# Optimization experiments

Hardware: AMD Instinct MI355X
Metric: run time of the kernel (lower is better)

## Reference

```python
import jax, jax.numpy as jnp
import numpy as np
from functools import partial

B, N = 4, 4096
WIDTH, HEADS, HD = 768, 12, 64
MINI, CONV_W = 16, 4
TTT_BASE_LR = 1.0
THETA = 10000.0
EPS = 1e-6


def _rope_table():
    half = HD // 2
    freqs = 1.0 / THETA ** (np.arange(0, HD, 2)[:half].astype(np.float32) / HD)
    t = np.arange(2 * MINI)
    f = np.outer(t, freqs).astype(np.float32)
    return jnp.asarray(np.cos(f)), jnp.asarray(np.sin(f))

_COS, _SIN = _rope_table()


def apply_rope(x, cos, sin):
    # x: [B,N,H,HD]; cos/sin: [N, HD//2]; pairs are (x[2i], x[2i+1])
    xe, xo = x[..., 0::2], x[..., 1::2]
    c, s = cos[None, :, None, :], sin[None, :, None, :]
    return jnp.stack([xe * c - xo * s, xe * s + xo * c], axis=-1).reshape(x.shape)


def ln_fwd(x, g, b):
    mu = x.mean(-1, keepdims=True)
    std = jnp.sqrt(x.var(-1, keepdims=True) + EPS)
    return g * ((x - mu) / std) + b


def ln_fused_l2_bwd(x, target, g, b):
    # grad of 0.5*||LN(x)-target||^2 w.r.t. x (official TTT fused form)
    D = x.shape[-1]
    mu = x.mean(-1, keepdims=True)
    std = jnp.sqrt(x.var(-1, keepdims=True) + EPS)
    x_hat = (x - mu) / std
    gxh = ((g * x_hat + b) - target) * g
    return (D * gxh - gxh.sum(-1, keepdims=True)
            - x_hat * (gxh * x_hat).sum(-1, keepdims=True)) / (D * std)


def causal_dwconv(x, kernel, bias):
    # depthwise causal conv: x [B,N,C], kernel [W,1,C], left-pad W-1
    y = jax.lax.conv_general_dilated(
        x, kernel, (1,), [(CONV_W - 1, 0)],
        dimension_numbers=('NWC', 'WIO', 'NWC'), feature_group_count=WIDTH)
    return y + bias


def _mini_step(ln_g, ln_b, carry, inp):
    W1, b1h = carry
    XQ, XK, XV, eta = inp  # [m,hd] x3, eta [m,m]
    Z1 = XK @ W1 + b1h
    grad = ln_fused_l2_bwd(Z1, XV - XK, ln_g, ln_b)
    Attn = jnp.tril(XQ @ XK.T)
    b1_bar = b1h - jnp.tril(eta) @ grad
    Z1_bar = XQ @ W1 - (eta * Attn) @ grad + b1_bar
    last_eta = eta[-1][:, None]
    W1_new = W1 - (last_eta * XK).T @ grad
    b1_new = b1h - jnp.sum(last_eta * grad, axis=0, keepdims=True)
    out = XQ + ln_fwd(Z1_bar, ln_g, ln_b)
    return (W1_new, b1_new), out


def ttt_forward(hidden_states, wq, wv, wo, wg,
                conv_q_kernel, conv_q_bias, conv_k_kernel, conv_k_bias,
                W1, b1, ttt_norm_scale, ttt_norm_bias,
                lr_kernel, lr_bias, learnable_token_idx,
                post_norm_scale, post_norm_bias):
    Bsz, Nlen, _ = hidden_states.shape
    xqk = hidden_states @ wq
    XV = hidden_states @ wv
    XQ = causal_dwconv(xqk, conv_q_kernel, conv_q_bias)
    XK = causal_dwconv(xqk, conv_k_kernel, conv_k_bias)
    XQ = XQ.reshape(Bsz, Nlen, HEADS, HD)
    XK = XK.reshape(Bsz, Nlen, HEADS, HD)
    XV = XV.reshape(Bsz, Nlen, HEADS, HD)

    pos = jnp.arange(Nlen) % MINI  # RoPE restarts each mini-batch (official)
    XQ = apply_rope(XQ, _COS[pos], _SIN[pos])
    XK = apply_rope(XK, _COS[pos], _SIN[pos])

    def to_mb(x):  # [B,N,H,hd] -> [B,H,n_mini,mini,hd]
        return x.reshape(Bsz, -1, MINI, HEADS, HD).transpose(0, 3, 1, 2, 4)
    XQ, XK, XV = to_mb(XQ), to_mb(XK), to_mb(XV)

    # learnable per-head, per-token learning rate -> eta [B,H,n_mini,mini,mini]
    X_mb = hidden_states.reshape(Bsz, -1, MINI, WIDTH)
    ttt_lr = jax.nn.sigmoid(jnp.einsum('bnmw,hw->bhnm', X_mb, lr_kernel[..., 0])
                            + lr_bias[None, :, None, :])
    ttt_lr = TTT_BASE_LR * ttt_lr / HD
    token_idx = jnp.maximum(1.0 / jnp.arange(1, MINI + 1, dtype=jnp.float32)
                            + learnable_token_idx, 0.0)
    eta = token_idx[None, None, None, :, None] * ttt_lr[:, :, :, None, :]

    def per_head(xq, xk, xv, e, w1, b1h, g, bln):
        step = partial(_mini_step, g, bln)
        _, out = jax.lax.scan(step, (w1, b1h), (xq, xk, xv, e))
        return out.reshape(-1, HD)  # [N, hd]

    per_batch = jax.vmap(per_head, in_axes=(0, 0, 0, 0, 0, 0, 0, 0))
    out = jax.vmap(per_batch, in_axes=(0, 0, 0, 0, None, None, None, None))(
        XQ, XK, XV, eta, W1, b1, ttt_norm_scale, ttt_norm_bias)  # [B,H,N,hd]
    out = out.transpose(0, 2, 1, 3).reshape(Bsz, Nlen, WIDTH)

    z = ln_fwd(out, post_norm_scale, post_norm_bias)  # post_norm
    gate = jax.nn.gelu(hidden_states @ wg)            # GLU gating
    return (gate * z) @ wo


def setup_inputs() -> dict:
    key = jax.random.key(0)
    ks = jax.random.split(key, 12)
    std = 0.02
    f32 = jnp.float32
    return {
        'hidden_states': jax.random.normal(ks[0], (B, N, WIDTH), f32),
        'wq': jax.random.normal(ks[1], (WIDTH, HEADS * HD), f32) * std,
        'wv': jax.random.normal(ks[2], (WIDTH, HEADS * HD), f32) * std,
        'wo': jax.random.normal(ks[3], (WIDTH, WIDTH), f32) * std,
        'wg': jax.random.normal(ks[4], (WIDTH, WIDTH), f32) * std,
        'conv_q_kernel': jax.random.normal(ks[5], (CONV_W, 1, WIDTH), f32) * 0.5,
        'conv_q_bias': jnp.zeros((WIDTH,), f32),
        'conv_k_kernel': jax.random.normal(ks[6], (CONV_W, 1, WIDTH), f32) * 0.5,
        'conv_k_bias': jnp.zeros((WIDTH,), f32),
        'W1': jax.random.normal(ks[7], (HEADS, HD, HD), f32) * std,
        'b1': jnp.zeros((HEADS, 1, HD), f32),
        'ttt_norm_scale': jnp.ones((HEADS, HD), f32),
        'ttt_norm_bias': jnp.zeros((HEADS, HD), f32),
        'lr_kernel': jax.random.normal(ks[8], (HEADS, WIDTH, 1), f32) * std,
        'lr_bias': jnp.zeros((HEADS, 1), f32),
        'learnable_token_idx': jax.random.normal(ks[9], (MINI,), f32) * 0.01,
        'post_norm_scale': jnp.ones((WIDTH,), f32),
        'post_norm_bias': jnp.zeros((WIDTH,), f32),
    }


def reference(hidden_states, wq, wv, wo, wg, conv_q_kernel, conv_q_bias,
              conv_k_kernel, conv_k_bias, W1, b1, ttt_norm_scale, ttt_norm_bias,
              lr_kernel, lr_bias, learnable_token_idx, post_norm_scale, post_norm_bias):
    return ttt_forward(hidden_states, wq, wv, wo, wg, conv_q_kernel, conv_q_bias,
                       conv_k_kernel, conv_k_bias, W1, b1, ttt_norm_scale,
                       ttt_norm_bias, lr_kernel, lr_bias, learnable_token_idx,
                       post_norm_scale, post_norm_bias)
```

## Files before the change

kernel.cpp:

```cpp
#include <hip/hip_runtime.h>
#include <math.h>

#define WIDTH 768
#define HEADS 12
#define HD 64
#define MINI 16
#define NSEQ 4096
#define BATCH 4
#define NMB (NSEQ/MINI)
#define EPS 1e-6f

typedef __attribute__((ext_vector_type(8))) short bf16x8;
typedef __attribute__((ext_vector_type(4))) float f32x4;
typedef __attribute__((ext_vector_type(4))) int   i32x4;

__device__ __forceinline__ float bfu2f(unsigned short h) {
    return __uint_as_float(((unsigned)h) << 16);
}
__device__ __forceinline__ void tsplit(float f, unsigned short& h, unsigned short& l) {
    unsigned uh = __float_as_uint(f) & 0xffff0000u;
    h = (unsigned short)(uh >> 16);
    l = (unsigned short)(__float_as_uint(f - __uint_as_float(uh)) >> 16);
}
__device__ __forceinline__ unsigned tpack(float f) {
    unsigned uh = __float_as_uint(f) & 0xffff0000u;
    return uh | (__float_as_uint(f - __uint_as_float(uh)) >> 16);
}
__device__ __forceinline__ void barrier_lgkm() {
    asm volatile("s_waitcnt lgkmcnt(0)\n\ts_barrier" ::: "memory");
}

struct ScanSM {
    unsigned sXKp[16 * 68];
    unsigned sGE[16 * 68];
    unsigned sCB[16 * 20];
    float    sU[64 * 68];
    float    sRedM[16 * 36];
    float    sRed3[16 * 36];
    float    sB1d[64];
};
struct GemmSM {
    unsigned short sAh[128 * 40], sAl[128 * 40];
    unsigned short sBh[128 * 40], sBl[128 * 40];
};
struct WtSM { float sT[64][65]; };
#define SMEM_BYTES 40960

__device__ void wtconv_body(char* smraw, int n0, int k0, const float* __restrict__ w,
                            unsigned short* __restrict__ hiT, unsigned short* __restrict__ loT)
{
    WtSM* W = (WtSM*)smraw;
    int t = threadIdx.x, r = t >> 2, cs = (t & 3) * 16;
#pragma unroll
    for (int i = 0; i < 16; i += 4)
        *(float4*)&W->sT[r][cs + i] = *(const float4*)&w[(size_t)(k0 + r) * WIDTH + n0 + cs + i];
    __syncthreads();
    ushort4 hb[4], lb[4];
#pragma unroll
    for (int i = 0; i < 16; i++) {
        unsigned short hh, ll;
        tsplit(W->sT[cs + i][r], hh, ll);
        ((unsigned short*)hb)[i] = hh;
        ((unsigned short*)lb)[i] = ll;
    }
#pragma unroll
    for (int i = 0; i < 4; i++) {
        *(ushort4*)&hiT[(size_t)(n0 + r) * WIDTH + k0 + cs + i * 4] = hb[i];
        *(ushort4*)&loT[(size_t)(n0 + r) * WIDTH + k0 + cs + i * 4] = lb[i];
    }
}

template<int ACT, int SPLITA>
__device__ void gemm_body(char* smraw, int by,
                          const float* __restrict__ Af,
                          const unsigned short* __restrict__ APh,
                          const unsigned short* __restrict__ APl,
                          const unsigned short* __restrict__ BhT,
                          const unsigned short* __restrict__ BlT,
                          float* __restrict__ C, int ldc, int K)
{
    GemmSM* g = (GemmSM*)smraw;
    const int tid = threadIdx.x;
    const int bm = by * 128;
    const int w = tid >> 6, lane = tid & 63, quad = lane >> 4, m16 = lane & 15;
    const int mw = (w & 1) * 64, nw = (w >> 1) * 64;
    const int srow = tid >> 1, sseg = (tid & 1) * 16;
    f32x4 acc[4][4];
#pragma unroll
    for (int a = 0; a < 4; a++)
#pragma unroll
        for (int c = 0; c < 4; c++) acc[a][c] = (f32x4){0.f, 0.f, 0.f, 0.f};

    for (int k0 = 0; k0 < K; k0 += 32) {
        uint4 vb0 = *(const uint4*)(BhT + (size_t)srow * K + k0 + sseg);
        uint4 vb1 = *(const uint4*)(BhT + (size_t)srow * K + k0 + sseg + 8);
        uint4 vd0 = *(const uint4*)(BlT + (size_t)srow * K + k0 + sseg);
        uint4 vd1 = *(const uint4*)(BlT + (size_t)srow * K + k0 + sseg + 8);
        if (SPLITA) {
            const float* Ap = Af + (size_t)(bm + srow) * K + k0 + sseg;
            float4 f0 = *(const float4*)(Ap);
            float4 f1 = *(const float4*)(Ap + 4);
            float4 f2 = *(const float4*)(Ap + 8);
            float4 f3 = *(const float4*)(Ap + 12);
            __syncthreads();
            unsigned short hs[16], ls[16];
            float fv[16] = {f0.x, f0.y, f0.z, f0.w, f1.x, f1.y, f1.z, f1.w,
                            f2.x, f2.y, f2.z, f2.w, f3.x, f3.y, f3.z, f3.w};
#pragma unroll
            for (int i = 0; i < 16; i++) tsplit(fv[i], hs[i], ls[i]);
            *(uint4*)&g->sAh[srow * 40 + sseg]     = *(uint4*)&hs[0];
            *(uint4*)&g->sAh[srow * 40 + sseg + 8] = *(uint4*)&hs[8];
            *(uint4*)&g->sAl[srow * 40 + sseg]     = *(uint4*)&ls[0];
            *(uint4*)&g->sAl[srow * 40 + sseg + 8] = *(uint4*)&ls[8];
        } else {
            uint4 va0 = *(const uint4*)(APh + (size_t)(bm + srow) * K + k0 + sseg);
            uint4 va1 = *(const uint4*)(APh + (size_t)(bm + srow) * K + k0 + sseg + 8);
            uint4 vc0 = *(const uint4*)(APl + (size_t)(bm + srow) * K + k0 + sseg);
            uint4 vc1 = *(const uint4*)(APl + (size_t)(bm + srow) * K + k0 + sseg + 8);
            __syncthreads();
            *(uint4*)&g->sAh[srow * 40 + sseg] = va0; *(uint4*)&g->sAh[srow * 40 + sseg + 8] = va1;
            *(uint4*)&g->sAl[srow * 40 + sseg] = vc0; *(uint4*)&g->sAl[srow * 40 + sseg + 8] = vc1;
        }
        *(uint4*)&g->sBh[srow * 40 + sseg] = vb0; *(uint4*)&g->sBh[srow * 40 + sseg + 8] = vb1;
        *(uint4*)&g->sBl[srow * 40 + sseg] = vd0; *(uint4*)&g->sBl[srow * 40 + sseg + 8] = vd1;
        __syncthreads();
        bf16x8 ah[4], al[4];
#pragma unroll
        for (int mt = 0; mt < 4; mt++) {
            ah[mt] = *(const bf16x8*)&g->sAh[(mw + mt * 16 + m16) * 40 + quad * 8];
            al[mt] = *(const bf16x8*)&g->sAl[(mw + mt * 16 + m16) * 40 + quad * 8];
        }
#pragma unroll
        for (int nt = 0; nt < 4; nt++) {
            bf16x8 bh8 = *(const bf16x8*)&g->sBh[(nw + nt * 16 + m16) * 40 + quad * 8];
            bf16x8 bl8 = *(const bf16x8*)&g->sBl[(nw + nt * 16 + m16) * 40 + quad * 8];
#pragma unroll
            for (int mt = 0; mt < 4; mt++) {
                acc[mt][nt] = __builtin_amdgcn_mfma_f32_16x16x32_bf16(ah[mt], bh8, acc[mt][nt], 0, 0, 0);
                acc[mt][nt] = __builtin_amdgcn_mfma_f32_16x16x32_bf16(al[mt], bh8, acc[mt][nt], 0, 0, 0);
                acc[mt][nt] = __builtin_amdgcn_mfma_f32_16x16x32_bf16(ah[mt], bl8, acc[mt][nt], 0, 0, 0);
            }
        }
    }
#pragma unroll
    for (int mt = 0; mt < 4; mt++)
#pragma unroll
        for (int nt = 0; nt < 4; nt++)
#pragma unroll
            for (int r = 0; r < 4; r++) {
                float v = acc[mt][nt][r];
                if (ACT == 1) {
                    float inner = 0.7978845608028654f * (v + 0.044715f * v * v * v);
                    v = 0.5f * v * (1.0f + tanhf(inner));
                }
                C[(size_t)(bm + mw + mt * 16 + quad * 4 + r) * ldc + nw + nt * 16 + m16] = v;
            }
}

__device__ void scan_body(char* smraw, int bh,
    const unsigned short* __restrict__ XQh, const unsigned short* __restrict__ XQl,
    const unsigned short* __restrict__ XKh, const unsigned short* __restrict__ XKl,
    const float* __restrict__ XVb, const float* __restrict__ lr_buf,
    const float* __restrict__ W1g, const float* __restrict__ b1g,
    const float* __restrict__ gln, const float* __restrict__ blnv,
    const float* __restrict__ lti, float* __restrict__ out)
{
    ScanSM* S = (ScanSM*)smraw;
    const int tid = threadIdx.x;
    const int w = tid >> 6, lane = tid & 63;
    const int quad = lane >> 4, m16 = lane & 15;
    const int b = bh / HEADS, h = bh - b * HEADS;
    const int jc = 16 * w + m16;
    const int j4 = 16 * w + quad * 4;

    float g4[4], b4[4], b1v[4], gg4[4];
#pragma unroll
    for (int r = 0; r < 4; r++) {
        g4[r] = gln[h * 64 + j4 + r];
        b4[r] = blnv[h * 64 + j4 + r];
        b1v[r] = b1g[h * 64 + j4 + r];
        gg4[r] = g4[r] * g4[r];
    }
    const float tok15 = fmaxf(1.0f / 16.0f + lti[15], 0.0f);
    float tki[4];
#pragma unroll
    for (int r = 0; r < 4; r++)
        tki[r] = fmaxf(1.0f / (float)(quad * 4 + r + 1) + lti[quad * 4 + r], 0.0f) / tok15;

    float ags = (gg4[0] + gg4[1]) + (gg4[2] + gg4[3]);
    ags += __shfl_xor(ags, 16); ags += __shfl_xor(ags, 32);
    if (lane == 0) S->sB1d[w] = ags;
    __syncthreads();
    const float Ag2 = S->sB1d[0] + S->sB1d[1] + S->sB1d[2] + S->sB1d[3];

    float W1f[2][8]; bf16x8 w1h[2], w1l[2];
#pragma unroll
    for (int kt = 0; kt < 2; kt++)
#pragma unroll
        for (int e = 0; e < 8; e++) {
            float f = W1g[h * 4096 + (kt * 32 + quad * 8 + e) * 64 + jc];
            W1f[kt][e] = f;
            unsigned short hh, ll; tsplit(f, hh, ll);
            w1h[kt][e] = (short)hh; w1l[kt][e] = (short)ll;
        }

    const unsigned short* xqh = XQh + (size_t)bh * NSEQ * 64;
    const unsigned short* xql = XQl + (size_t)bh * NSEQ * 64;
    const unsigned short* xkh = XKh + (size_t)bh * NSEQ * 64;
    const unsigned short* xkl = XKl + (size_t)bh * NSEQ * 64;
    const float* xvB = XVb + (size_t)b * NSEQ * WIDTH + h * 64;
    const float* lrB = lr_buf + (size_t)bh * NSEQ;
    float* outB = out + (size_t)b * NSEQ * WIDTH + h * 64;

    bf16x8 ones8;
#pragma unroll
    for (int e = 0; e < 8; e++) ones8[e] = (short)0x3F80;
    const bf16x8 zf = {0, 0, 0, 0, 0, 0, 0, 0};

    bf16x8 pqh[2], pql[2], pkh[2], pkl[2];
    float4 pxv; ushort4 pth, ptl, poh, pol; float plr;
    {
        const size_t tok = m16;
#pragma unroll
        for (int kt = 0; kt < 2; kt++) {
            pqh[kt] = *(const bf16x8*)(xqh + tok * 64 + kt * 32 + quad * 8);
            pql[kt] = *(const bf16x8*)(xql + tok * 64 + kt * 32 + quad * 8);
            pkh[kt] = *(const bf16x8*)(xkh + tok * 64 + kt * 32 + quad * 8);
            pkl[kt] = *(const bf16x8*)(xkl + tok * 64 + kt * 32 + quad * 8);
        }
        pxv = *(const float4*)(xvB + tok * WIDTH + j4);
        pth = *(const ushort4*)(xkh + tok * 64 + j4);
        ptl = *(const ushort4*)(xkl + tok * 64 + j4);
        poh = *(const ushort4*)(xqh + tok * 64 + j4);
        pol = *(const ushort4*)(xql + tok * 64 + j4);
        plr = lrB[m16];
    }

    for (int s = 0; s < NMB; s++) {
        bf16x8 qh[2] = {pqh[0], pqh[1]}, ql[2] = {pql[0], pql[1]};
        bf16x8 kh[2] = {pkh[0], pkh[1]}, kl[2] = {pkl[0], pkl[1]};
        float xv4[4] = {pxv.x, pxv.y, pxv.z, pxv.w};
        float xkt4[4], xqo4[4];
        xkt4[0] = bfu2f(pth.x) + bfu2f(ptl.x); xkt4[1] = bfu2f(pth.y) + bfu2f(ptl.y);
        xkt4[2] = bfu2f(pth.z) + bfu2f(ptl.z); xkt4[3] = bfu2f(pth.w) + bfu2f(ptl.w);
        xqo4[0] = bfu2f(poh.x) + bfu2f(pol.x); xqo4[1] = bfu2f(poh.y) + bfu2f(pol.y);
        xqo4[2] = bfu2f(poh.z) + bfu2f(pol.z); xqo4[3] = bfu2f(poh.w) + bfu2f(pol.w);
        const float lrc = plr;
        const float sc = tok15 * lrc;

#pragma unroll
        for (int kt = 0; kt < 2; kt++) {
            i32x4 p0, p1;
#pragma unroll
            for (int e = 0; e < 4; e++)
                p0[e] = (int)((((unsigned)(unsigned short)kh[kt][e]) << 16) | (unsigned short)kl[kt][e]);
#pragma unroll
            for (int e = 0; e < 4; e++)
                p1[e] = (int)((((unsigned)(unsigned short)kh[kt][4 + e]) << 16) | (unsigned short)kl[kt][4 + e]);
            *(i32x4*)&S->sXKp[m16 * 68 + kt * 32 + quad * 8] = p0;
            *(i32x4*)&S->sXKp[m16 * 68 + kt * 32 + quad * 8 + 4] = p1;
        }

        {
            const int sn = (s + 1 < NMB) ? s + 1 : s;
            const size_t tok = (size_t)sn * 16 + m16;
#pragma unroll
            for (int kt = 0; kt < 2; kt++) {
                pqh[kt] = *(const bf16x8*)(xqh + tok * 64 + kt * 32 + quad * 8);
                pql[kt] = *(const bf16x8*)(xql + tok * 64 + kt * 32 + quad * 8);
                pkh[kt] = *(const bf16x8*)(xkh + tok * 64 + kt * 32 + quad * 8);
                pkl[kt] = *(const bf16x8*)(xkl + tok * 64 + kt * 32 + quad * 8);
            }
            pxv = *(const float4*)(xvB + tok * WIDTH + j4);
            pth = *(const ushort4*)(xkh + tok * 64 + j4);
            ptl = *(const ushort4*)(xkl + tok * 64 + j4);
            poh = *(const ushort4*)(xqh + tok * 64 + j4);
            pol = *(const ushort4*)(xql + tok * 64 + j4);
            plr = lrB[(size_t)sn * 16 + m16];
        }

        f32x4 z1 = {0.f, 0.f, 0.f, 0.f}, zq = {0.f, 0.f, 0.f, 0.f};
#pragma unroll
        for (int kt = 0; kt < 2; kt++) {
            z1 = __builtin_amdgcn_mfma_f32_16x16x32_bf16(w1h[kt], kh[kt], z1, 0, 0, 0);
            z1 = __builtin_amdgcn_mfma_f32_16x16x32_bf16(w1h[kt], kl[kt], z1, 0, 0, 0);
            z1 = __builtin_amdgcn_mfma_f32_16x16x32_bf16(w1l[kt], kh[kt], z1, 0, 0, 0);
            zq = __builtin_amdgcn_mfma_f32_16x16x32_bf16(w1h[kt], qh[kt], zq, 0, 0, 0);
            zq = __builtin_amdgcn_mfma_f32_16x16x32_bf16(w1h[kt], ql[kt], zq, 0, 0, 0);
            zq = __builtin_amdgcn_mfma_f32_16x16x32_bf16(w1l[kt], qh[kt], zq, 0, 0, 0);
        }
        f32x4 at = {0.f, 0.f, 0.f, 0.f};
        if (w == 3) {
#pragma unroll
            for (int kt = 0; kt < 2; kt++) {
                at = __builtin_amdgcn_mfma_f32_16x16x32_bf16(qh[kt], kh[kt], at, 0, 0, 0);
                at = __builtin_amdgcn_mfma_f32_16x16x32_bf16(qh[kt], kl[kt], at, 0, 0, 0);
                at = __builtin_amdgcn_mfma_f32_16x16x32_bf16(ql[kt], kh[kt], at, 0, 0, 0);
            }
        }
#pragma unroll
        for (int r = 0; r < 4; r++) z1[r] += b1v[r];

        float c1g[4];
        float s1 = 0.f, s2 = 0.f, a1 = 0.f, a4 = 0.f, a3 = 0.f, a5 = 0.f;
#pragma unroll
        for (int r = 0; r < 4; r++) {
            float z = z1[r];
            float t = xv4[r] - xkt4[r];
            c1g[r] = (b4[r] - t) * g4[r];
            s1 += z; s2 += z * z;
            float gz = gg4[r] * z;
            a1 += gz; a4 += gz * z;
            a3 += c1g[r]; a5 += c1g[r] * z;
        }
        s1 += __shfl_xor(s1, 16); s2 += __shfl_xor(s2, 16);
        a1 += __shfl_xor(a1, 16); a4 += __shfl_xor(a4, 16);
        a3 += __shfl_xor(a3, 16); a5 += __shfl_xor(a5, 16);
        s1 += __shfl_xor(s1, 32); s2 += __shfl_xor(s2, 32);
        a1 += __shfl_xor(a1, 32); a4 += __shfl_xor(a4, 32);
        a3 += __shfl_xor(a3, 32); a5 += __shfl_xor(a5, 32);
        if (quad == 0) {
            *(float4*)&S->sRedM[m16 * 36 + w * 8]     = make_float4(s1, s2, a1, a4);
            *(float4*)&S->sRedM[m16 * 36 + w * 8 + 4] = make_float4(a3, a5, 0.f, 0.f);
        }
        if (w == 3) {
            i32x4 cw;
#pragma unroll
            for (int r = 0; r < 4; r++) {
                float v = (m16 <= quad * 4 + r) ? -(tki[r] * (1.0f + at[r])) : 0.0f;
                cw[r] = (int)tpack(v);
            }
            *(i32x4*)&S->sCB[m16 * 20 + quad * 4] = cw;
        }
        barrier_lgkm();

        float S1 = 0.f, S2 = 0.f, A1 = 0.f, A4 = 0.f, A3 = 0.f, A5 = 0.f;
#pragma unroll
        for (int w2 = 0; w2 < 4; w2++) {
            float4 pa = *(const float4*)&S->sRedM[m16 * 36 + w2 * 8];
            float4 pb = *(const float4*)&S->sRedM[m16 * 36 + w2 * 8 + 4];
            S1 += pa.x; S2 += pa.y; A1 += pa.z; A4 += pa.w;
            A3 += pb.x; A5 += pb.y;
        }
        float mu = S1 * (1.0f / 64.0f);
        float var = S2 * (1.0f / 64.0f) - mu * mu;
        float rstd = rsqrtf(var + EPS);
        float T1 = rstd * (A1 - mu * Ag2) + A3;
        float T2 = rstd * rstd * (A4 - 2.0f * mu * A1 + mu * mu * Ag2)
                 + rstd * (A5 - mu * A3);
        i32x4 gw;
#pragma unroll
        for (int r = 0; r < 4; r++) {
            float xh = (z1[r] - mu) * rstd;
            float gxh = gg4[r] * xh + c1g[r];
            float grad = (64.0f * gxh - T1 - xh * T2) * (rstd * (1.0f / 64.0f));
            gw[r] = (int)tpack(sc * grad);
        }
        *(i32x4*)&S->sGE[m16 * 68 + j4] = gw;
        barrier_lgkm();

        bf16x8 akh8 = zf, akl8 = zf;
#pragma unroll
        for (int e = 0; e < 8; e++) {
            unsigned u = (quad < 2) ? S->sXKp[(quad * 8 + e) * 68 + 16 * w + m16] : 0u;
            akh8[e] = (short)(u >> 16); akl8[e] = (short)(u & 0xffffu);
        }
        bf16x8 agh = zf, agl = zf;
#pragma unroll
        for (int nt = 0; nt < 4; nt++) {
            bf16x8 gh8 = zf, gl8 = zf;
#pragma unroll
            for (int e = 0; e < 8; e++) {
                unsigned u = (quad < 2) ? S->sGE[(quad * 8 + e) * 68 + 16 * nt + m16] : 0u;
                gh8[e] = (short)(u >> 16); gl8[e] = (short)(u & 0xffffu);
            }
            if (nt == w) { agh = gh8; agl = gl8; }
            f32x4 ua = {0.f, 0.f, 0.f, 0.f};
            ua = __builtin_amdgcn_mfma_f32_16x16x32_bf16(akh8, gh8, ua, 0, 0, 0);
            ua = __builtin_amdgcn_mfma_f32_16x16x32_bf16(akl8, gh8, ua, 0, 0, 0);
            ua = __builtin_amdgcn_mfma_f32_16x16x32_bf16(akh8, gl8, ua, 0, 0, 0);
#pragma unroll
            for (int r = 0; r < 4; r++)
                S->sU[(16 * w + quad * 4 + r) * 68 + 16 * nt + m16] = ua[r];
            if (w == 1) {
                f32x4 bda = {0.f, 0.f, 0.f, 0.f};
                bda = __builtin_amdgcn_mfma_f32_16x16x32_bf16(ones8, gh8, bda, 0, 0, 0);
                bda = __builtin_amdgcn_mfma_f32_16x16x32_bf16(ones8, gl8, bda, 0, 0, 0);
                if (quad == 0) S->sB1d[16 * nt + m16] = bda[0];
            }
        }
        bf16x8 cbh = zf, cbl = zf;
#pragma unroll
        for (int e = 0; e < 8; e++) {
            unsigned u = (quad < 2) ? S->sCB[(quad * 8 + e) * 20 + m16] : 0u;
            cbh[e] = (short)(u >> 16); cbl[e] = (short)(u & 0xffffu);
        }
        zq = __builtin_amdgcn_mfma_f32_16x16x32_bf16(agh, cbh, zq, 0, 0, 0);
        zq = __builtin_amdgcn_mfma_f32_16x16x32_bf16(agl, cbh, zq, 0, 0, 0);
        zq = __builtin_amdgcn_mfma_f32_16x16x32_bf16(agh, cbl, zq, 0, 0, 0);
        float zb[4];
#pragma unroll
        for (int r = 0; r < 4; r++) zb[r] = zq[r] + b1v[r];
        float u1p = (zb[0] + zb[1]) + (zb[2] + zb[3]);
        float u2p = (zb[0] * zb[0] + zb[1] * zb[1]) + (zb[2] * zb[2] + zb[3] * zb[3]);
        u1p += __shfl_xor(u1p, 16); u2p += __shfl_xor(u2p, 16);
        u1p += __shfl_xor(u1p, 32); u2p += __shfl_xor(u2p, 32);
        if (quad == 0) *(float2*)&S->sRed3[m16 * 36 + w * 8] = make_float2(u1p, u2p);
        barrier_lgkm();

        float V1 = 0.f, V2 = 0.f;
#pragma unroll
        for (int w2 = 0; w2 < 4; w2++) {
            float2 p = *(const float2*)&S->sRed3[m16 * 36 + w2 * 8];
            V1 += p.x; V2 += p.y;
        }
        float mu2 = V1 * (1.0f / 64.0f);
        float va2 = V2 * (1.0f / 64.0f) - mu2 * mu2;
        float rs2 = rsqrtf(va2 + EPS);
        float4 ov;
        ov.x = xqo4[0] + fmaf(g4[0], (zb[0] - mu2) * rs2, b4[0]);
        ov.y = xqo4[1] + fmaf(g4[1], (zb[1] - mu2) * rs2, b4[1]);
        ov.z = xqo4[2] + fmaf(g4[2], (zb[2] - mu2) * rs2, b4[2]);
        ov.w = xqo4[3] + fmaf(g4[3], (zb[3] - mu2) * rs2, b4[3]);
        *(float4*)&outB[(size_t)(s * 16 + m16) * WIDTH + j4] = ov;

#pragma unroll
        for (int kt = 0; kt < 2; kt++)
#pragma unroll
            for (int e = 0; e < 8; e++) {
                float f = W1f[kt][e] - S->sU[(kt * 32 + quad * 8 + e) * 68 + jc];
                W1f[kt][e] = f;
                unsigned short hh, ll; tsplit(f, hh, ll);
                w1h[kt][e] = (short)hh; w1l[kt][e] = (short)ll;
            }
        float4 bdv = *(const float4*)&S->sB1d[j4];
        b1v[0] -= bdv.x; b1v[1] -= bdv.y; b1v[2] -= bdv.z; b1v[3] -= bdv.w;
    }
}

__global__ __launch_bounds__(256, 2)
void mega_kernel(const unsigned short* __restrict__ XQh, const unsigned short* __restrict__ XQl,
                 const unsigned short* __restrict__ XKh, const unsigned short* __restrict__ XKl,
                 const float* __restrict__ XVb, const float* __restrict__ lrbuf,
                 const float* __restrict__ W1, const float* __restrict__ b1,
                 const float* __restrict__ tns, const float* __restrict__ tnb,
                 const float* __restrict__ lti, float* __restrict__ ttto,
                 const float* __restrict__ wo, unsigned short* __restrict__ woThi,
                 unsigned short* __restrict__ woTlo,
                 const float* __restrict__ hidden, const unsigned short* __restrict__ wTgh,
                 const unsigned short* __restrict__ wTgl, float* __restrict__ gate)
{
    __shared__ __align__(16) char sm[SMEM_BYTES];
    int bid = blockIdx.x;
    if (bid < 48) {
        scan_body(sm, bid, XQh, XQl, XKh, XKl, XVb, lrbuf, W1, b1, tns, tnb, lti, ttto);
    } else if (bid < 192) {
        int idx = bid - 48;
        wtconv_body(sm, (idx % 12) * 64, (idx / 12) * 64, wo, woThi, woTlo);
    } else {
        int idx = bid - 192;
        int bx = idx % 6, by = idx / 6;
        int bn = bx * 128;
        gemm_body<1, 1>(sm, by, hidden, nullptr, nullptr,
                        wTgh + (size_t)bn * WIDTH, wTgl + (size_t)bn * WIDTH,
                        gate + bn, WIDTH, WIDTH);
    }
}

__global__ __launch_bounds__(256, 2)
void gemm_qv_kernel(const float* __restrict__ hidden,
                    const unsigned short* __restrict__ wThi, const unsigned short* __restrict__ wTlo,
                    float* __restrict__ xqk, float* __restrict__ XVb)
{
    __shared__ __align__(16) char sm[SMEM_BYTES];
    int bn = blockIdx.x * 128;
    float* C = (bn < WIDTH) ? (xqk + bn) : (XVb + bn - WIDTH);
    gemm_body<0, 1>(sm, blockIdx.y, hidden, nullptr, nullptr,
                    wThi + (size_t)bn * WIDTH, wTlo + (size_t)bn * WIDTH, C, WIDTH, WIDTH);
}

__global__ __launch_bounds__(256, 2)
void gemm_out_kernel(const unsigned short* __restrict__ gzh, const unsigned short* __restrict__ gzl,
                     const unsigned short* __restrict__ woThi, const unsigned short* __restrict__ woTlo,
                     float* __restrict__ out)
{
    __shared__ __align__(16) char sm[SMEM_BYTES];
    int bn = blockIdx.x * 128;
    gemm_body<0, 0>(sm, blockIdx.y, nullptr, gzh, gzl,
                    woThi + (size_t)bn * WIDTH, woTlo + (size_t)bn * WIDTH, out + bn, WIDTH, WIDTH);
}

__global__ __launch_bounds__(256)
void wtconv3_kernel(const float* __restrict__ wq, const float* __restrict__ wv,
                    const float* __restrict__ wg,
                    unsigned short* __restrict__ hiT, unsigned short* __restrict__ loT)
{
    __shared__ __align__(16) char sm[sizeof(WtSM)];
    int widx = blockIdx.z;
    const float* src = (widx == 0) ? wq : ((widx == 1) ? wv : wg);
    size_t off = (size_t)widx * WIDTH * WIDTH;
    wtconv_body(sm, blockIdx.x * 64, blockIdx.y * 64, src, hiT + off, loT + off);
}

__global__ __launch_bounds__(384)
void conv_rope_kernel(const float* __restrict__ xqk,
                      const float* __restrict__ kq, const float* __restrict__ bq,
                      const float* __restrict__ kk, const float* __restrict__ bk,
                      unsigned short* __restrict__ XQh, unsigned short* __restrict__ XQl,
                      unsigned short* __restrict__ XKh, unsigned short* __restrict__ XKl)
{
    int bid = blockIdx.x;
    int n = bid & (NSEQ - 1);
    int b = bid >> 12;
    int p = threadIdx.x;
    int c = p * 2;
    int pp = p & 31;
    float qe = bq[c], qo = bq[c + 1], ke = bk[c], ko = bk[c + 1];
#pragma unroll
    for (int w = 0; w < 4; w++) {
        int nn = n - 3 + w;
        if (nn >= 0) {
            const float* xr = xqk + ((size_t)(bid - n + nn)) * WIDTH + c;
            float xe = xr[0], xo = xr[1];
            qe = fmaf(xe, kq[w * WIDTH + c], qe);
            qo = fmaf(xo, kq[w * WIDTH + c + 1], qo);
            ke = fmaf(xe, kk[w * WIDTH + c], ke);
            ko = fmaf(xo, kk[w * WIDTH + c + 1], ko);
        }
    }
    int pos = n & (MINI - 1);
    float freq = expf(-(float)pp * (9.210340371976184f / 32.0f));
    float ang = (float)pos * freq;
    float c_ = cosf(ang), s_ = sinf(ang);
    int hh = p >> 5;
    int cc = pp * 2;
    size_t o = ((size_t)(b * HEADS + hh) * NSEQ + n) * 64 + cc;
    float q0 = qe * c_ - qo * s_, q1 = qe * s_ + qo * c_;
    float k0 = ke * c_ - ko * s_, k1 = ke * s_ + ko * c_;
    ushort2 h2, l2;
    tsplit(q0, h2.x, l2.x); tsplit(q1, h2.y, l2.y);
    *(ushort2*)&XQh[o] = h2; *(ushort2*)&XQl[o] = l2;
    tsplit(k0, h2.x, l2.x); tsplit(k1, h2.y, l2.y);
    *(ushort2*)&XKh[o] = h2; *(ushort2*)&XKl[o] = l2;
}

__global__ __launch_bounds__(256)
void lr_kernel(const float* __restrict__ hidden, const float* __restrict__ lrk,
               const float* __restrict__ lrb, float* __restrict__ lr_buf)
{
    int wave = threadIdx.x >> 6;
    int lane = threadIdx.x & 63;
    int row = blockIdx.x * 4 + wave;
    int b = row >> 12;
    int n = row & (NSEQ - 1);
    const float* hr = hidden + (size_t)row * WIDTH;
    float hv[12];
#pragma unroll
    for (int t = 0; t < 12; t++) hv[t] = hr[lane + 64 * t];
    for (int h = 0; h < HEADS; h++) {
        const float* lk = lrk + h * WIDTH;
        float acc = 0.f;
#pragma unroll
        for (int t = 0; t < 12; t++) acc = fmaf(hv[t], lk[lane + 64 * t], acc);
#pragma unroll
        for (int m = 1; m < 64; m <<= 1) acc += __shfl_xor(acc, m);
        if (lane == 0) {
            float s = 1.0f / (1.0f + __expf(-(acc + lrb[h])));
            lr_buf[((size_t)(b * HEADS + h)) * NSEQ + n] = s * (1.0f / HD);
        }
    }
}

__global__ __launch_bounds__(256)
void postgate_kernel(const float* __restrict__ tout, const float* __restrict__ gate,
                     const float* __restrict__ ps, const float* __restrict__ pb,
                     unsigned short* __restrict__ gzh, unsigned short* __restrict__ gzl)
{
    __shared__ float red[8];
    int row = blockIdx.x;
    int tid = threadIdx.x;
    const float* x = tout + (size_t)row * WIDTH;
    float v[3];
    float s1 = 0, s2 = 0;
#pragma unroll
// ... 80 lines not shown
```

Before: 1.163 ms.

## Run each TTT scan head on a single wavefront to remove block barriers

The sequential mini-batch scan for each (batch, head) now runs on one 64-lane wavefront instead of four waves splitting the 64 output columns. Each lane holds all four column tiles of W1 in registers and performs the full LN reductions with shuffles, so the per-step cross-wave LDS reductions and block barriers become plain lgkmcnt waits. MFMA sections are given higher scheduling priority, and the mega kernel's launch bounds drop to one block per SM. The trade-off is four times more MFMA and VALU work per wave on the serial critical path, much higher register pressure that may cause spills, and lower occupancy for the co-scheduled GEMM and weight-conversion blocks.

```diff
diff --git a/kernel.cpp b/kernel.cpp
--- a/kernel.cpp
+++ b/kernel.cpp
@@ -26,17 +26,16 @@
     unsigned uh = __float_as_uint(f) & 0xffff0000u;
     return uh | (__float_as_uint(f - __uint_as_float(uh)) >> 16);
 }
-__device__ __forceinline__ void barrier_lgkm() {
-    asm volatile("s_waitcnt lgkmcnt(0)\n\ts_barrier" ::: "memory");
-}
-
-struct ScanSM {
+__device__ __forceinline__ void fence_lds() {
+    asm volatile("s_waitcnt lgkmcnt(0)" ::: "memory");
+    __builtin_amdgcn_sched_barrier(0);
+}
+
+struct ScanSM1 {
     unsigned sXKp[16 * 68];
     unsigned sGE[16 * 68];
     unsigned sCB[16 * 20];
-    float    sU[64 * 68];
-    float    sRedM[16 * 36];
-    float    sRed3[16 * 36];
+    float    sUw[64 * 68];
     float    sB1d[64];
 };
 struct GemmSM {
@@ -46,11 +45,11 @@
 struct WtSM { float sT[64][65]; };
 #define SMEM_BYTES 40960
 
-__device__ void wtconv_body(char* smraw, int n0, int k0, const float* __restrict__ w,
+__device__ void wtconv_body(char* smraw, int tid, int n0, int k0, const float* __restrict__ w,
                             unsigned short* __restrict__ hiT, unsigned short* __restrict__ loT)
 {
     WtSM* W = (WtSM*)smraw;
-    int t = threadIdx.x, r = t >> 2, cs = (t & 3) * 16;
+    int t = tid, r = t >> 2, cs = (t & 3) * 16;
 #pragma unroll
     for (int i = 0; i < 16; i += 4)
         *(float4*)&W->sT[r][cs + i] = *(const float4*)&w[(size_t)(k0 + r) * WIDTH + n0 + cs + i];
@@ -71,7 +70,7 @@
 }
 
 template<int ACT, int SPLITA>
-__device__ void gemm_body(char* smraw, int by,
+__device__ void gemm_body(char* smraw, int tid, int by,
                           const float* __restrict__ Af,
                           const unsigned short* __restrict__ APh,
                           const unsigned short* __restrict__ APl,
@@ -80,7 +79,6 @@
                           float* __restrict__ C, int ldc, int K)
 {
     GemmSM* g = (GemmSM*)smraw;
-    const int tid = threadIdx.x;
     const int bm = by * 128;
     const int w = tid >> 6, lane = tid & 63, quad = lane >> 4, m16 = lane & 15;
     const int mw = (w & 1) * 64, nw = (w >> 1) * 64;
@@ -157,7 +155,7 @@
             }
 }
 
-__device__ void scan_body(char* smraw, int bh,
+__device__ void scan_wave(char* smraw, int lane, int bh,
     const unsigned short* __restrict__ XQh, const unsigned short* __restrict__ XQl,
     const unsigned short* __restrict__ XKh, const unsigned short* __restrict__ XKl,
     const float* __restrict__ XVb, const float* __restrict__ lr_buf,
@@ -165,44 +163,46 @@
     const float* __restrict__ gln, const float* __restrict__ blnv,
     const float* __restrict__ lti, float* __restrict__ out)
 {
-    ScanSM* S = (ScanSM*)smraw;
-    const int tid = threadIdx.x;
-    const int w = tid >> 6, lane = tid & 63;
+    ScanSM1* S = (ScanSM1*)smraw;
     const int quad = lane >> 4, m16 = lane & 15;
     const int b = bh / HEADS, h = bh - b * HEADS;
-    const int jc = 16 * w + m16;
-    const int j4 = 16 * w + quad * 4;
-
-    float g4[4], b4[4], b1v[4], gg4[4];
-#pragma unroll
-    for (int r = 0; r < 4; r++) {
-        g4[r] = gln[h * 64 + j4 + r];
-        b4[r] = blnv[h * 64 + j4 + r];
-        b1v[r] = b1g[h * 64 + j4 + r];
-        gg4[r] = g4[r] * g4[r];
-    }
+
+    float g4[4][4], b4[4][4], gg4[4][4], b1v[4][4];
+#pragma unroll
+    for (int jt = 0; jt < 4; jt++)
+#pragma unroll
+        for (int r = 0; r < 4; r++) {
+            int j = 16 * jt + quad * 4 + r;
+            g4[jt][r] = gln[h * 64 + j];
+            b4[jt][r] = blnv[h * 64 + j];
+            b1v[jt][r] = b1g[h * 64 + j];
+            gg4[jt][r] = g4[jt][r] * g4[jt][r];
+        }
     const float tok15 = fmaxf(1.0f / 16.0f + lti[15], 0.0f);
     float tki[4];
 #pragma unroll
     for (int r = 0; r < 4; r++)
         tki[r] = fmaxf(1.0f / (float)(quad * 4 + r + 1) + lti[quad * 4 + r], 0.0f) / tok15;
 
-    float ags = (gg4[0] + gg4[1]) + (gg4[2] + gg4[3]);
+    float ags = 0.f;
+#pragma unroll
+    for (int jt = 0; jt < 4; jt++)
+        ags += (gg4[jt][0] + gg4[jt][1]) + (gg4[jt][2] + gg4[jt][3]);
     ags += __shfl_xor(ags, 16); ags += __shfl_xor(ags, 32);
-    if (lane == 0) S->sB1d[w] = ags;
-    __syncthreads();
-    const float Ag2 = S->sB1d[0] + S->sB1d[1] + S->sB1d[2] + S->sB1d[3];
-
-    float W1f[2][8]; bf16x8 w1h[2], w1l[2];
-#pragma unroll
-    for (int kt = 0; kt < 2; kt++)
-#pragma unroll
-        for (int e = 0; e < 8; e++) {
-            float f = W1g[h * 4096 + (kt * 32 + quad * 8 + e) * 64 + jc];
-            W1f[kt][e] = f;
-            unsigned short hh, ll; tsplit(f, hh, ll);
-            w1h[kt][e] = (short)hh; w1l[kt][e] = (short)ll;
-        }
+    const float Ag2 = ags;
+
+    float W1f[4][2][8]; bf16x8 w1h[4][2], w1l[4][2];
+#pragma unroll
+    for (int jt = 0; jt < 4; jt++)
+#pragma unroll
+        for (int kt = 0; kt < 2; kt++)
+#pragma unroll
+            for (int e = 0; e < 8; e++) {
+                float f = W1g[h * 4096 + (kt * 32 + quad * 8 + e) * 64 + 16 * jt + m16];
+                W1f[jt][kt][e] = f;
+                unsigned short hh, ll; tsplit(f, hh, ll);
+                w1h[jt][kt][e] = (short)hh; w1l[jt][kt][e] = (short)ll;
+            }
 
     const unsigned short* xqh = XQh + (size_t)bh * NSEQ * 64;
     const unsigned short* xql = XQl + (size_t)bh * NSEQ * 64;
@@ -215,10 +215,9 @@
     bf16x8 ones8;
 #pragma unroll
     for (int e = 0; e < 8; e++) ones8[e] = (short)0x3F80;
-    const bf16x8 zf = {0, 0, 0, 0, 0, 0, 0, 0};
 
     bf16x8 pqh[2], pql[2], pkh[2], pkl[2];
-    float4 pxv; ushort4 pth, ptl, poh, pol; float plr;
+    float4 pxv[4]; ushort4 pth[4], ptl[4]; float plr;
     {
         const size_t tok = m16;
 #pragma unroll
@@ -228,25 +227,29 @@
             pkh[kt] = *(const bf16x8*)(xkh + tok * 64 + kt * 32 + quad * 8);
             pkl[kt] = *(const bf16x8*)(xkl + tok * 64 + kt * 32 + quad * 8);
         }
-        pxv = *(const float4*)(xvB + tok * WIDTH + j4);
-        pth = *(const ushort4*)(xkh + tok * 64 + j4);
-        ptl = *(const ushort4*)(xkl + tok * 64 + j4);
-        poh = *(const ushort4*)(xqh + tok * 64 + j4);
-        pol = *(const ushort4*)(xql + tok * 64 + j4);
+#pragma unroll
+        for (int jt = 0; jt < 4; jt++) {
+            pxv[jt] = *(const float4*)(xvB + tok * WIDTH + 16 * jt + quad * 4);
+            pth[jt] = *(const ushort4*)(xkh + tok * 64 + 16 * jt + quad * 4);
+            ptl[jt] = *(const ushort4*)(xkl + tok * 64 + 16 * jt + quad * 4);
+        }
         plr = lrB[m16];
     }
 
     for (int s = 0; s < NMB; s++) {
         bf16x8 qh[2] = {pqh[0], pqh[1]}, ql[2] = {pql[0], pql[1]};
         bf16x8 kh[2] = {pkh[0], pkh[1]}, kl[2] = {pkl[0], pkl[1]};
-        float xv4[4] = {pxv.x, pxv.y, pxv.z, pxv.w};
-        float xkt4[4], xqo4[4];
-        xkt4[0] = bfu2f(pth.x) + bfu2f(ptl.x); xkt4[1] = bfu2f(pth.y) + bfu2f(ptl.y);
-        xkt4[2] = bfu2f(pth.z) + bfu2f(ptl.z); xkt4[3] = bfu2f(pth.w) + bfu2f(ptl.w);
-        xqo4[0] = bfu2f(poh.x) + bfu2f(pol.x); xqo4[1] = bfu2f(poh.y) + bfu2f(pol.y);
-        xqo4[2] = bfu2f(poh.z) + bfu2f(pol.z); xqo4[3] = bfu2f(poh.w) + bfu2f(pol.w);
-        const float lrc = plr;
-        const float sc = tok15 * lrc;
+        float xv[4][4], xkt[4][4];
+#pragma unroll
+        for (int jt = 0; jt < 4; jt++) {
+            xv[jt][0] = pxv[jt].x; xv[jt][1] = pxv[jt].y;
+            xv[jt][2] = pxv[jt].z; xv[jt][3] = pxv[jt].w;
+            xkt[jt][0] = bfu2f(pth[jt].x) + bfu2f(ptl[jt].x);
+            xkt[jt][1] = bfu2f(pth[jt].y) + bfu2f(ptl[jt].y);
+            xkt[jt][2] = bfu2f(pth[jt].z) + bfu2f(ptl[jt].z);
+            xkt[jt][3] = bfu2f(pth[jt].w) + bfu2f(ptl[jt].w);
+        }
+        const float sc = tok15 * plr;
 
 #pragma unroll
         for (int kt = 0; kt < 2; kt++) {
@@ -271,59 +274,87 @@
                 pkh[kt] = *(const bf16x8*)(xkh + tok * 64 + kt * 32 + quad * 8);
                 pkl[kt] = *(const bf16x8*)(xkl + tok * 64 + kt * 32 + quad * 8);
             }
-            pxv = *(const float4*)(xvB + tok * WIDTH + j4);
-            pth = *(const ushort4*)(xkh + tok * 64 + j4);
-            ptl = *(const ushort4*)(xkl + tok * 64 + j4);
-            poh = *(const ushort4*)(xqh + tok * 64 + j4);
-            pol = *(const ushort4*)(xql + tok * 64 + j4);
+#pragma unroll
+            for (int jt = 0; jt < 4; jt++) {
+                pxv[jt] = *(const float4*)(xvB + tok * WIDTH + 16 * jt + quad * 4);
+                pth[jt] = *(const ushort4*)(xkh + tok * 64 + 16 * jt + quad * 4);
+                ptl[jt] = *(const ushort4*)(xkl + tok * 64 + 16 * jt + quad * 4);
+            }
             plr = lrB[(size_t)sn * 16 + m16];
         }
-
-        f32x4 z1 = {0.f, 0.f, 0.f, 0.f}, zq = {0.f, 0.f, 0.f, 0.f};
+        ushort4 qoh[4], qol[4];
+        {
+            const size_t tokc = (size_t)s * 16 + m16;
+#pragma unroll
+            for (int jt = 0; jt < 4; jt++) {
+                qoh[jt] = *(const ushort4*)(xqh + tokc * 64 + 16 * jt + quad * 4);
+                qol[jt] = *(const ushort4*)(xql + tokc * 64 + 16 * jt + quad * 4);
+            }
+        }
+
+        f32x4 z1[4], zq[4];
+#pragma unroll
+        for (int jt = 0; jt < 4; jt++) { z1[jt] = (f32x4){0.f,0.f,0.f,0.f}; zq[jt] = (f32x4){0.f,0.f,0.f,0.f}; }
+        f32x4 at = {0.f, 0.f, 0.f, 0.f};
+        __builtin_amdgcn_s_setprio(1);
 #pragma unroll
         for (int kt = 0; kt < 2; kt++) {
-            z1 = __builtin_amdgcn_mfma_f32_16x16x32_bf16(w1h[kt], kh[kt], z1, 0, 0, 0);
-            z1 = __builtin_amdgcn_mfma_f32_16x16x32_bf16(w1h[kt], kl[kt], z1, 0, 0, 0);
-            z1 = __builtin_amdgcn_mfma_f32_16x16x32_bf16(w1l[kt], kh[kt], z1, 0, 0, 0);
-            zq = __builtin_amdgcn_mfma_f32_16x16x32_bf16(w1h[kt], qh[kt], zq, 0, 0, 0);
-            zq = __builtin_amdgcn_mfma_f32_16x16x32_bf16(w1h[kt], ql[kt], zq, 0, 0, 0);
-            zq = __builtin_amdgcn_mfma_f32_16x16x32_bf16(w1l[kt], qh[kt], zq, 0, 0, 0);
-        }
-        f32x4 at = {0.f, 0.f, 0.f, 0.f};
-        if (w == 3) {
-#pragma unroll
-            for (int kt = 0; kt < 2; kt++) {
-                at = __builtin_amdgcn_mfma_f32_16x16x32_bf16(qh[kt], kh[kt], at, 0, 0, 0);
-                at = __builtin_amdgcn_mfma_f32_16x16x32_bf16(qh[kt], kl[kt], at, 0, 0, 0);
-                at = __builtin_amdgcn_mfma_f32_16x16x32_bf16(ql[kt], kh[kt], at, 0, 0, 0);
-            }
-        }
-#pragma unroll
-        for (int r = 0; r < 4; r++) z1[r] += b1v[r];
-
-        float c1g[4];
+#pragma unroll
+            for (int jt = 0; jt < 4; jt++) {
+                z1[jt] = __builtin_amdgcn_mfma_f32_16x16x32_bf16(w1h[jt][kt], kh[kt], z1[jt], 0, 0, 0);
+                z1[jt] = __builtin_amdgcn_mfma_f32_16x16x32_bf16(w1h[jt][kt], kl[kt], z1[jt], 0, 0, 0);
+                z1[jt] = __builtin_amdgcn_mfma_f32_16x16x32_bf16(w1l[jt][kt], kh[kt], z1[jt], 0, 0, 0);
+                zq[jt] = __builtin_amdgcn_mfma_f32_16x16x32_bf16(w1h[jt][kt], qh[kt], zq[jt], 0, 0, 0);
+                zq[jt] = __builtin_amdgcn_mfma_f32_16x16x32_bf16(w1h[jt][kt], ql[kt], zq[jt], 0, 0, 0);
+                zq[jt] = __builtin_amdgcn_mfma_f32_16x16x32_bf16(w1l[jt][kt], qh[kt], zq[jt], 0, 0, 0);
+            }
+            at = __builtin_amdgcn_mfma_f32_16x16x32_bf16(qh[kt], kh[kt], at, 0, 0, 0);
+            at = __builtin_amdgcn_mfma_f32_16x16x32_bf16(qh[kt], kl[kt], at, 0, 0, 0);
+            at = __builtin_amdgcn_mfma_f32_16x16x32_bf16(ql[kt], kh[kt], at, 0, 0, 0);
+        }
+        __builtin_amdgcn_s_setprio(0);
+
+        float c1g[4][4];
         float s1 = 0.f, s2 = 0.f, a1 = 0.f, a4 = 0.f, a3 = 0.f, a5 = 0.f;
 #pragma unroll
-        for (int r = 0; r < 4; r++) {
-            float z = z1[r];
-            float t = xv4[r] - xkt4[r];
-            c1g[r] = (b4[r] - t) * g4[r];
-            s1 += z; s2 += z * z;
-            float gz = gg4[r] * z;
-            a1 += gz; a4 += gz * z;
-            a3 += c1g[r]; a5 += c1g[r] * z;
-        }
+        for (int jt = 0; jt < 4; jt++)
+#pragma unroll
+            for (int r = 0; r < 4; r++) {
+                float z = z1[jt][r] + b1v[jt][r];
+                z1[jt][r] = z;
+                float t = xv[jt][r] - xkt[jt][r];
+                c1g[jt][r] = (b4[jt][r] - t) * g4[jt][r];
+                s1 += z; s2 += z * z;
+                float gz = gg4[jt][r] * z;
+                a1 += gz; a4 += gz * z;
+                a3 += c1g[jt][r]; a5 += c1g[jt][r] * z;
+            }
         s1 += __shfl_xor(s1, 16); s2 += __shfl_xor(s2, 16);
         a1 += __shfl_xor(a1, 16); a4 += __shfl_xor(a4, 16);
         a3 += __shfl_xor(a3, 16); a5 += __shfl_xor(a5, 16);
         s1 += __shfl_xor(s1, 32); s2 += __shfl_xor(s2, 32);
         a1 += __shfl_xor(a1, 32); a4 += __shfl_xor(a4, 32);
         a3 += __shfl_xor(a3, 32); a5 += __shfl_xor(a5, 32);
-        if (quad == 0) {
-            *(float4*)&S->sRedM[m16 * 36 + w * 8]     = make_float4(s1, s2, a1, a4);
-            *(float4*)&S->sRedM[m16 * 36 + w * 8 + 4] = make_float4(a3, a5, 0.f, 0.f);
-        }
-        if (w == 3) {
+
+        float mu = s1 * (1.0f / 64.0f);
+        float var = s2 * (1.0f / 64.0f) - mu * mu;
+        float rstd = rsqrtf(var + EPS);
+        float T1 = rstd * (a1 - mu * Ag2) + a3;
+        float T2 = rstd * rstd * (a4 - 2.0f * mu * a1 + mu * mu * Ag2)
+                 + rstd * (a5 - mu * a3);
+#pragma unroll
+        for (int jt = 0; jt < 4; jt++) {
+            i32x4 gw;
+#pragma unroll
+            for (int r = 0; r < 4; r++) {
+                float xh = (z1[jt][r] - mu) * rstd;
+                float gxh = gg4[jt][r] * xh + c1g[jt][r];
+                float grad = (64.0f * gxh - T1 - xh * T2) * (rstd * (1.0f / 64.0f));
+                gw[r] = (int)tpack(sc * grad);
+            }
+            *(i32x4*)&S->sGE[m16 * 68 + 16 * jt + quad * 4] = gw;
+        }
+        {
             i32x4 cw;
 #pragma unroll
             for (int r = 0; r < 4; r++) {
@@ -332,113 +363,107 @@
             }
             *(i32x4*)&S->sCB[m16 * 20 + quad * 4] = cw;
         }
-        barrier_lgkm();
-
-        float S1 = 0.f, S2 = 0.f, A1 = 0.f, A4 = 0.f, A3 = 0.f, A5 = 0.f;
-#pragma unroll
-        for (int w2 = 0; w2 < 4; w2++) {
-            float4 pa = *(const float4*)&S->sRedM[m16 * 36 + w2 * 8];
-            float4 pb = *(const float4*)&S->sRedM[m16 * 36 + w2 * 8 + 4];
-            S1 += pa.x; S2 += pa.y; A1 += pa.z; A4 += pa.w;
-            A3 += pb.x; A5 += pb.y;
-        }
-        float mu = S1 * (1.0f / 64.0f);
-        float var = S2 * (1.0f / 64.0f) - mu * mu;
-        float rstd = rsqrtf(var + EPS);
-        float T1 = rstd * (A1 - mu * Ag2) + A3;
-        float T2 = rstd * rstd * (A4 - 2.0f * mu * A1 + mu * mu * Ag2)
-                 + rstd * (A5 - mu * A3);
-        i32x4 gw;
-#pragma unroll
-        for (int r = 0; r < 4; r++) {
-            float xh = (z1[r] - mu) * rstd;
-            float gxh = gg4[r] * xh + c1g[r];
-            float grad = (64.0f * gxh - T1 - xh * T2) * (rstd * (1.0f / 64.0f));
-            gw[r] = (int)tpack(sc * grad);
-        }
-        *(i32x4*)&S->sGE[m16 * 68 + j4] = gw;
-        barrier_lgkm();
-
-        bf16x8 akh8 = zf, akl8 = zf;
-#pragma unroll
-        for (int e = 0; e < 8; e++) {
-            unsigned u = (quad < 2) ? S->sXKp[(quad * 8 + e) * 68 + 16 * w + m16] : 0u;
-            akh8[e] = (short)(u >> 16); akl8[e] = (short)(u & 0xffffu);
-        }
-        bf16x8 agh = zf, agl = zf;
-#pragma unroll
-        for (int nt = 0; nt < 4; nt++) {
-            bf16x8 gh8 = zf, gl8 = zf;
+        fence_lds();
+
+        bf16x8 gh[4], gl[4], cbh, cbl;
+#pragma unroll
+        for (int jt = 0; jt < 4; jt++) {
 #pragma unroll
             for (int e = 0; e < 8; e++) {
-                unsigned u = (quad < 2) ? S->sGE[(quad * 8 + e) * 68 + 16 * nt + m16] : 0u;
-                gh8[e] = (short)(u >> 16); gl8[e] = (short)(u & 0xffffu);
-            }
-            if (nt == w) { agh = gh8; agl = gl8; }
-            f32x4 ua = {0.f, 0.f, 0.f, 0.f};
-            ua = __builtin_amdgcn_mfma_f32_16x16x32_bf16(akh8, gh8, ua, 0, 0, 0);
-            ua = __builtin_amdgcn_mfma_f32_16x16x32_bf16(akl8, gh8, ua, 0, 0, 0);
-            ua = __builtin_amdgcn_mfma_f32_16x16x32_bf16(akh8, gl8, ua, 0, 0, 0);
-#pragma unroll
-            for (int r = 0; r < 4; r++)
-                S->sU[(16 * w + quad * 4 + r) * 68 + 16 * nt + m16] = ua[r];
-            if (w == 1) {
-                f32x4 bda = {0.f, 0.f, 0.f, 0.f};
-                bda = __builtin_amdgcn_mfma_f32_16x16x32_bf16(ones8, gh8, bda, 0, 0, 0);
-                bda = __builtin_amdgcn_mfma_f32_16x16x32_bf16(ones8, gl8, bda, 0, 0, 0);
-                if (quad == 0) S->sB1d[16 * nt + m16] = bda[0];
-            }
-        }
-        bf16x8 cbh = zf, cbl = zf;
+                unsigned u = (quad < 2) ? S->sGE[(quad * 8 + e) * 68 + 16 * jt + m16] : 0u;
+                gh[jt][e] = (short)(u >> 16); gl[jt][e] = (short)(u & 0xffffu);
+            }
+        }
 #pragma unroll
         for (int e = 0; e < 8; e++) {
             unsigned u = (quad < 2) ? S->sCB[(quad * 8 + e) * 20 + m16] : 0u;
             cbh[e] = (short)(u >> 16); cbl[e] = (short)(u & 0xffffu);
         }
-        zq = __builtin_amdgcn_mfma_f32_16x16x32_bf16(agh, cbh, zq, 0, 0, 0);
-        zq = __builtin_amdgcn_mfma_f32_16x16x32_bf16(agl, cbh, zq, 0, 0, 0);
-        zq = __builtin_amdgcn_mfma_f32_16x16x32_bf16(agh, cbl, zq, 0, 0, 0);
-        float zb[4];
-#pragma unroll
-        for (int r = 0; r < 4; r++) zb[r] = zq[r] + b1v[r];
-        float u1p = (zb[0] + zb[1]) + (zb[2] + zb[3]);
-        float u2p = (zb[0] * zb[0] + zb[1] * zb[1]) + (zb[2] * zb[2] + zb[3] * zb[3]);
-        u1p += __shfl_xor(u1p, 16); u2p += __shfl_xor(u2p, 16);
-        u1p += __shfl_xor(u1p, 32); u2p += __shfl_xor(u2p, 32);
-        if (quad == 0) *(float2*)&S->sRed3[m16 * 36 + w * 8] = make_float2(u1p, u2p);
-        barrier_lgkm();
-
-        float V1 = 0.f, V2 = 0.f;
-#pragma unroll
-        for (int w2 = 0; w2 < 4; w2++) {
-            float2 p = *(const float2*)&S->sRed3[m16 * 36 + w2 * 8];
-            V1 += p.x; V2 += p.y;
-        }
-        float mu2 = V1 * (1.0f / 64.0f);
-        float va2 = V2 * (1.0f / 64.0f) - mu2 * mu2;
+
+        __builtin_amdgcn_s_setprio(1);
+#pragma unroll
+        for (int kr = 0; kr < 4; kr++) {
+            bf16x8 akh8, akl8;
+#pragma unroll
+            for (int e = 0; e < 8; e++) {
+                unsigned u = (quad < 2) ? S->sXKp[(quad * 8 + e) * 68 + 16 * kr + m16] : 0u;
+                akh8[e] = (short)(u >> 16); akl8[e] = (short)(u & 0xffffu);
+            }
+#pragma unroll
+            for (int jt = 0; jt < 4; jt++) {
+                f32x4 ua = {0.f, 0.f, 0.f, 0.f};
+                ua = __builtin_amdgcn_mfma_f32_16x16x32_bf16(akh8, gh[jt], ua, 0, 0, 0);
+                ua = __builtin_amdgcn_mfma_f32_16x16x32_bf16(akl8, gh[jt], ua, 0, 0, 0);
+                ua = __builtin_amdgcn_mfma_f32_16x16x32_bf16(akh8, gl[jt], ua, 0, 0, 0);
+                *(f32x4*)&S->sUw[(16 * jt + m16) * 68 + 16 * kr + quad * 4] = ua;
+            }
+        }
+#pragma unroll
+        for (int jt = 0; jt < 4; jt++) {
+            zq[jt] = __builtin_amdgcn_mfma_f32_16x16x32_bf16(gh[jt], cbh, zq[jt], 0, 0, 0);
+            zq[jt] = __builtin_amdgcn_mfma_f32_16x16x32_bf16(gl[jt], cbh, zq[jt], 0, 0, 0);
+            zq[jt] = __builtin_amdgcn_mfma_f32_16x16x32_bf16(gh[jt], cbl, zq[jt], 0, 0, 0);
+            f32x4 bda = {0.f, 0.f, 0.f, 0.f};
+            bda = __builtin_amdgcn_mfma_f32_16x16x32_bf16(ones8, gh[jt], bda, 0, 0, 0);
+            bda = __builtin_amdgcn_mfma_f32_16x16x32_bf16(ones8, gl[jt], bda, 0, 0, 0);
+            if (quad == 0) S->sB1d[16 * jt + m16] = bda[0];
+        }
+        __builtin_amdgcn_s_setprio(0);
+
+        float zb[4][4]; float u1 = 0.f, u2 = 0.f;
+#pragma unroll
+        for (int jt = 0; jt < 4; jt++)
+#pragma unroll
+            for (int r = 0; r < 4; r++) {
+                float z = zq[jt][r] + b1v[jt][r];
+                zb[jt][r] = z; u1 += z; u2 += z * z;
+            }
+        u1 += __shfl_xor(u1, 16); u2 += __shfl_xor(u2, 16);
+        u1 += __shfl_xor(u1, 32); u2 += __shfl_xor(u2, 32);
+        float mu2 = u1 * (1.0f / 64.0f);
+        float va2 = u2 * (1.0f / 64.0f) - mu2 * mu2;
         float rs2 = rsqrtf(va2 + EPS);
-        float4 ov;
-        ov.x = xqo4[0] + fmaf(g4[0], (zb[0] - mu2) * rs2, b4[0]);
-        ov.y = xqo4[1] + fmaf(g4[1], (zb[1] - mu2) * rs2, b4[1]);
-        ov.z = xqo4[2] + fmaf(g4[2], (zb[2] - mu2) * rs2, b4[2]);
-        ov.w = xqo4[3] + fmaf(g4[3], (zb[3] - mu2) * rs2, b4[3]);
-        *(float4*)&outB[(size_t)(s * 16 + m16) * WIDTH + j4] = ov;
-
-#pragma unroll
-        for (int kt = 0; kt < 2; kt++)
-#pragma unroll
-            for (int e = 0; e < 8; e++) {
-                float f = W1f[kt][e] - S->sU[(kt * 32 + quad * 8 + e) * 68 + jc];
-                W1f[kt][e] = f;
-                unsigned short hh, ll; tsplit(f, hh, ll);
-                w1h[kt][e] = (short)hh; w1l[kt][e] = (short)ll;
-            }
-        float4 bdv = *(const float4*)&S->sB1d[j4];
-        b1v[0] -= bdv.x; b1v[1] -= bdv.y; b1v[2] -= bdv.z; b1v[3] -= bdv.w;
-    }
-}
-
-__global__ __launch_bounds__(256, 2)
+#pragma unroll
+        for (int jt = 0; jt < 4; jt++) {
+            float4 ov;
+            ov.x = (bfu2f(qoh[jt].x) + bfu2f(qol[jt].x)) + fmaf(g4[jt][0], (zb[jt][0] - mu2) * rs2, b4[jt][0]);
+            ov.y = (bfu2f(qoh[jt].y) + bfu2f(qol[jt].y)) + fmaf(g4[jt][1], (zb[jt][1] - mu2) * rs2, b4[jt][1]);
+            ov.z = (bfu2f(qoh[jt].z) + bfu2f(qol[jt].z)) + fmaf(g4[jt][2], (zb[jt][2] - mu2) * rs2, b4[jt][2]);
+            ov.w = (bfu2f(qoh[jt].w) + bfu2f(qol[jt].w)) + fmaf(g4[jt][3], (zb[jt][3] - mu2) * rs2, b4[jt][3]);
+            *(float4*)&outB[(size_t)(s * 16 + m16) * WIDTH + 16 * jt + quad * 4] = ov;
+        }
+
+        fence_lds();
+
+#pragma unroll
+        for (int jt = 0; jt < 4; jt++) {
+#pragma unroll
+            for (int kt = 0; kt < 2; kt++) {
+                f32x4 u0 = *(const f32x4*)&S->sUw[(16 * jt + m16) * 68 + 32 * kt + quad * 8];
+                f32x4 u1v = *(const f32x4*)&S->sUw[(16 * jt + m16) * 68 + 32 * kt + quad * 8 + 4];
+#pragma unroll
+                for (int e = 0; e < 4; e++) {
+                    float f = W1f[jt][kt][e] - u0[e];
+                    W1f[jt][kt][e] = f;
+                    unsigned short hh, ll; tsplit(f, hh, ll);
+                    w1h[jt][kt][e] = (short)hh; w1l[jt][kt][e] = (short)ll;
+                }
+#pragma unroll
+                for (int e = 0; e < 4; e++) {
+                    float f = W1f[jt][kt][4 + e] - u1v[e];
+                    W1f[jt][kt][4 + e] = f;
+                    unsigned short hh, ll; tsplit(f, hh, ll);
+                    w1h[jt][kt][4 + e] = (short)hh; w1l[jt][kt][4 + e] = (short)ll;
+                }
+            }
+            float4 bdv = *(const float4*)&S->sB1d[16 * jt + quad * 4];
+            b1v[jt][0] -= bdv.x; b1v[jt][1] -= bdv.y;
+            b1v[jt][2] -= bdv.z; b1v[jt][3] -= bdv.w;
+        }
+    }
+}
+
+__global__ __launch_bounds__(256, 1)
 void mega_kernel(const unsigned short* __restrict__ XQh, const unsigned short* __restrict__ XQl,
                  const unsigned short* __restrict__ XKh, const unsigned short* __restrict__ XKl,
                  const float* __restrict__ XVb, const float* __restrict__ lrbuf,
@@ -453,15 +478,18 @@
     __shared__ __align__(16) char sm[SMEM_BYTES];
     int bid = blockIdx.x;
     if (bid < 48) {
-        scan_body(sm, bid, XQh, XQl, XKh, XKl, XVb, lrbuf, W1, b1, tns, tnb, lti, ttto);
+        if (threadIdx.x < 64)
+            scan_wave(sm, threadIdx.x, bid, XQh, XQl, XKh, XKl, XVb, lrbuf,
+                      W1, b1, tns, tnb, lti, ttto);
+        return;
     } else if (bid < 192) {
         int idx = bid - 48;
-        wtconv_body(sm, (idx % 12) * 64, (idx / 12) * 64, wo, woThi, woTlo);
+        wtconv_body(sm, threadIdx.x, (idx % 12) * 64, (idx / 12) * 64, wo, woThi, woTlo);
     } else {
         int idx = bid - 192;
         int bx = idx % 6, by = idx / 6;
         int bn = bx * 128;
-        gemm_body<1, 1>(sm, by, hidden, nullptr, nullptr,
+        gemm_body<1, 1>(sm, threadIdx.x, by, hidden, nullptr, nullptr,
                         wTgh + (size_t)bn * WIDTH, wTgl + (size_t)bn * WIDTH,
                         gate + bn, WIDTH, WIDTH);
     }
@@ -475,7 +503,7 @@
     __shared__ __align__(16) char sm[SMEM_BYTES];
     int bn = blockIdx.x * 128;
     float* C = (bn < WIDTH) ? (xqk + bn) : (XVb + bn - WIDTH);
-    gemm_body<0, 1>(sm, blockIdx.y, hidden, nullptr, nullptr,
+    gemm_body<0, 1>(sm, threadIdx.x, blockIdx.y, hidden, nullptr, nullptr,
                     wThi + (size_t)bn * WIDTH, wTlo + (size_t)bn * WIDTH, C, WIDTH, WIDTH);
 }
 
@@ -486,7 +514,7 @@
 {
     __shared__ __align__(16) char sm[SMEM_BYTES];
     int bn = blockIdx.x * 128;
-    gemm_body<0, 0>(sm, blockIdx.y, nullptr, gzh, gzl,
+    gemm_body<0, 0>(sm, threadIdx.x, blockIdx.y, nullptr, gzh, gzl,
                     woThi + (size_t)bn * WIDTH, woTlo + (size_t)bn * WIDTH, out + bn, WIDTH, WIDTH);
 }
 
@@ -499,7 +527,7 @@
     int widx = blockIdx.z;
     const float* src = (widx == 0) ? wq : ((widx == 1) ? wv : wg);
     size_t off = (size_t)widx * WIDTH * WIDTH;
-    wtconv_body(sm, blockIdx.x * 64, blockIdx.y * 64, src, hiT + off, loT + off);
+    wtconv_body(sm, threadIdx.x, blockIdx.x * 64, blockIdx.y * 64, src, hiT + off, loT + off);
 }
 
 __global__ __launch_bounds__(384)
```

After: 1.553 ms. 33.5% more time.
